# Kernel tuning notes

Measured on AMD Instinct MI355X. Metric: run time of the kernel, lower is better.

## Reference

```python
import jax, jax.numpy as jnp
import numpy as np

N, E = 50000, 800000
DIN, DOUT, DIM, K = 64, 64, 3, 8
EPS_GMM = 1e-15
BN_EPS = 1e-5
ALPHA = 0.01


def setup_inputs() -> dict:
    key = jax.random.key(0)
    ks = jax.random.split(key, 10)
    x = jax.random.normal(ks[0], (N, DIN), dtype=jnp.float32)
    edge_idx = jax.random.randint(ks[1], (2, E), 0, N, dtype=jnp.int64)
    edge_attr = jax.random.uniform(ks[2], (E, DIM), dtype=jnp.float32)
    # GMMConv params (PyG: g maps in -> K*out, lin is root weight, plus bias)
    W_g = jax.random.normal(ks[3], (DIN, K * DOUT), dtype=jnp.float32) * (1.0 / np.sqrt(DIN))
    mu = jax.random.normal(ks[4], (K, DIM), dtype=jnp.float32)
    sigma = jnp.ones((K, DIM), dtype=jnp.float32) + 0.1 * jax.random.normal(ks[5], (K, DIM), dtype=jnp.float32)
    W_root = jax.random.normal(ks[6], (DIN, DOUT), dtype=jnp.float32) * (1.0 / np.sqrt(DIN))
    bias = jnp.zeros((DOUT,), dtype=jnp.float32)
    gamma = jnp.ones((DOUT,), dtype=jnp.float32)
    beta = jnp.zeros((DOUT,), dtype=jnp.float32)
    return {"x": x, "edge_idx": edge_idx, "edge_attr": edge_attr,
            "W_g": W_g, "mu": mu, "sigma": sigma, "W_root": W_root,
            "bias": bias, "gamma": gamma, "beta": beta}


def reference(x, edge_idx, edge_attr, W_g, mu, sigma, W_root, bias, gamma, beta):
    src, dst = edge_idx[0], edge_idx[1]
    # Gaussian mixture edge weights: [E, K]
    diff = edge_attr[:, None, :] - mu[None, :, :]              # [E, K, DIM]
    gauss = jnp.exp((-0.5 * diff * diff / (EPS_GMM + sigma[None] ** 2)).sum(-1))  # [E, K]
    # Transform node features once: [N, K, DOUT]
    x_trans = (x @ W_g).reshape(N, K, DOUT)
    # Per-edge message: weighted sum over kernels of gathered source features
    msg = jnp.einsum('ekm,ek->em', x_trans[src], gauss)        # [E, DOUT]
    # Mean-aggregate to destination nodes
    agg = jax.ops.segment_sum(msg, dst, num_segments=N)        # [N, DOUT]
    cnt = jax.ops.segment_sum(jnp.ones((E,), dtype=x.dtype), dst, num_segments=N)
    agg = agg / jnp.maximum(cnt, 1.0)[:, None]
    # Root weight + bias
    out = agg + x @ W_root + bias
    # BatchNorm1d (training mode: batch stats, biased variance)
    m = out.mean(axis=0)
    v = ((out - m) ** 2).mean(axis=0)
    out = gamma * (out - m) * jax.lax.rsqrt(v + BN_EPS) + beta
    # LeakyReLU
    return jnp.where(out > 0, out, ALPHA * out)
```

## Files before the change

kernel.cpp:

```cpp
#include <hip/hip_runtime.h>
#include <hip/hip_bf16.h>

#define N_NODES 50000
#define N_EDGES 800000

__device__ __forceinline__ void store_val(float* p, float v) { *p = v; }
__device__ __forceinline__ void store_val(__hip_bfloat16* p, float v) { *p = __float2bfloat16(v); }
__device__ __forceinline__ float load_val(const float* p) { return *p; }
__device__ __forceinline__ float load_val(const __hip_bfloat16* p) { return __bfloat162float(*p); }

__global__ void prep_c1_kernel(const float* __restrict__ sigma, float* __restrict__ c1) {
    int i = threadIdx.x;
    if (i < 24) {
        float s = sigma[i];
        c1[i] = -0.5f / (s * s + 1e-15f);
    }
}

template <typename T>
__global__ void gemm_xt_kernel(const float* __restrict__ x, const float* __restrict__ Wg,
                               T* __restrict__ xt) {
    __shared__ float xs[16][64];
    const int tid = threadIdx.x;
    const int row0 = blockIdx.x << 4;
    for (int i = tid; i < 1024; i += 256) xs[i >> 6][i & 63] = x[(size_t)row0 * 64 + i];
    __syncthreads();

    float acc0[16], acc1[16];
#pragma unroll
    for (int r = 0; r < 16; r++) { acc0[r] = 0.f; acc1[r] = 0.f; }

#pragma unroll 4
    for (int i = 0; i < 64; i++) {
        float w0 = Wg[i * 512 + tid];
        float w1 = Wg[i * 512 + tid + 256];
#pragma unroll
        for (int r = 0; r < 16; r++) {
            float xv = xs[r][i];
            acc0[r] = fmaf(xv, w0, acc0[r]);
            acc1[r] = fmaf(xv, w1, acc1[r]);
        }
    }
#pragma unroll
    for (int r = 0; r < 16; r++) {
        size_t o = ((size_t)(row0 + r)) * 512 + tid;
        store_val(&xt[o], acc0[r]);
        store_val(&xt[o + 256], acc1[r]);
    }
}

template <typename T>
__global__ void edge_kernel(const int* __restrict__ eidx, const float* __restrict__ eattr,
                            const float* __restrict__ mu, const float* __restrict__ c1,
                            const T* __restrict__ xt, float* __restrict__ agg,
                            float* __restrict__ cnt) {
    __shared__ float smu[24], sc1[24];
    const int tid = threadIdx.x;
    if (tid < 24) smu[tid] = mu[tid];
    else if (tid < 48) sc1[tid - 24] = c1[tid - 24];
    __syncthreads();

    const int e = (blockIdx.x << 2) + (tid >> 6);
    const int lane = tid & 63;

    const int src = eidx[e];
    const int dst = eidx[N_EDGES + e];

    const float a0 = eattr[e * 3 + 0];
    const float a1 = eattr[e * 3 + 1];
    const float a2 = eattr[e * 3 + 2];

    const int kk = lane & 7;
    const float d0 = a0 - smu[kk * 3 + 0];
    const float d1 = a1 - smu[kk * 3 + 1];
    const float d2 = a2 - smu[kk * 3 + 2];
    const float gv = __expf(fmaf(d0 * d0, sc1[kk * 3 + 0],
                            fmaf(d1 * d1, sc1[kk * 3 + 1],
                                 d2 * d2 * sc1[kk * 3 + 2])));

    const T* xr = xt + (size_t)src * 512 + lane;
    float xv[8];
#pragma unroll
    for (int k = 0; k < 8; k++) xv[k] = load_val(&xr[k * 64]);

    float v = 0.f;
#pragma unroll
    for (int k = 0; k < 8; k++) {
        float gk = __shfl(gv, k, 64);
        v = fmaf(gk, xv[k], v);
    }

    atomicAdd(&agg[(size_t)dst * 64 + lane], v);
    if (lane == 0) atomicAdd(&cnt[dst], 1.0f);
}

__global__ void root_stats_kernel(const float* __restrict__ x, const float* __restrict__ Wr,
                                  const float* __restrict__ bias, const float* __restrict__ agg,
                                  const float* __restrict__ cnt, float* __restrict__ out_pre,
                                  double* __restrict__ colsum, double* __restrict__ colsumsq) {
    __shared__ float wr[4096];
    __shared__ float rs[256], rsq[256];
    for (int i = threadIdx.x; i < 4096; i += 256) wr[i] = Wr[i];
    __syncthreads();

    const int wave = threadIdx.x >> 6;
    const int lane = threadIdx.x & 63;
    const float b = bias[lane];
    const int stride = gridDim.x * 4;

    float s = 0.f, sq = 0.f;
    for (int n = blockIdx.x * 4 + wave; n < N_NODES; n += stride) {
        float xv = x[(size_t)n * 64 + lane];
        float acc = 0.f;
#pragma unroll
        for (int i = 0; i < 64; i++)
            acc = fmaf(__shfl(xv, i, 64), wr[i * 64 + lane], acc);
        float c = cnt[n];
        float val = agg[(size_t)n * 64 + lane] / fmaxf(c, 1.f) + acc + b;
        out_pre[(size_t)n * 64 + lane] = val;
        s += val;
        sq += val * val;
    }

    rs[threadIdx.x] = s;
    rsq[threadIdx.x] = sq;
    __syncthreads();
    if (threadIdx.x < 64) {
        float ts = rs[threadIdx.x] + rs[threadIdx.x + 64] + rs[threadIdx.x + 128] + rs[threadIdx.x + 192];
        float tq = rsq[threadIdx.x] + rsq[threadIdx.x + 64] + rsq[threadIdx.x + 128] + rsq[threadIdx.x + 192];
        atomicAdd(&colsum[threadIdx.x], (double)ts);
        atomicAdd(&colsumsq[threadIdx.x], (double)tq);
    }
}

__global__ void bn_prep_kernel(const double* __restrict__ colsum, const double* __restrict__ colsumsq,
                               float* __restrict__ meanr) {
    int c = threadIdx.x;
    if (c < 64) {
        double m = colsum[c] / (double)N_NODES;
        double var = colsumsq[c] / (double)N_NODES - m * m;
        meanr[c] = (float)m;
        meanr[64 + c] = (float)(1.0 / sqrt(var + 1e-5));
    }
}

__global__ void finalize_kernel(float* __restrict__ out, const float* __restrict__ meanr,
                                const float* __restrict__ gamma, const float* __restrict__ beta) {
    const int i = blockIdx.x * 256 + threadIdx.x;
    const int c = i & 63;
    float v = out[i];
    float o = fmaf((v - meanr[c]) * meanr[64 + c], gamma[c], beta[c]);
    out[i] = o > 0.f ? o : 0.01f * o;
}

extern "C" void kernel_launch(void* const* d_in, const int* in_sizes, int n_in,
                              void* d_out, int out_size, void* d_ws, size_t ws_size,
                              hipStream_t stream) {
    const float* x     = (const float*)d_in[0];
    const int*   eidx  = (const int*)d_in[1];
    const float* eattr = (const float*)d_in[2];
    const float* Wg    = (const float*)d_in[3];
    const float* mu    = (const float*)d_in[4];
    const float* sigma = (const float*)d_in[5];
    const float* Wr    = (const float*)d_in[6];
    const float* bias  = (const float*)d_in[7];
    const float* gamma = (const float*)d_in[8];
    const float* beta  = (const float*)d_in[9];
    float* out = (float*)d_out;

    char* ws = (char*)d_ws;
    const size_t agg_off     = 0;
    const size_t cnt_off     = agg_off + (size_t)N_NODES * 64 * 4;
    const size_t colsum_off  = cnt_off + (size_t)N_NODES * 4;
    const size_t colsumsq_off = colsum_off + 64 * 8;
    const size_t meanr_off   = colsumsq_off + 64 * 8;
    const size_t c1_off      = meanr_off + 128 * 4;
    const size_t xt_off      = c1_off + 128;
    const size_t zero_bytes  = colsumsq_off + 512;

    float*  agg      = (float*)(ws + agg_off);
    float*  cnt      = (float*)(ws + cnt_off);
    double* colsum   = (double*)(ws + colsum_off);
    double* colsumsq = (double*)(ws + colsumsq_off);
    float*  meanr    = (float*)(ws + meanr_off);
    float*  c1       = (float*)(ws + c1_off);

    hipMemsetAsync(ws + agg_off, 0, zero_bytes, stream);
    prep_c1_kernel<<<1, 32, 0, stream>>>(sigma, c1);

    const bool f32path = ws_size >= xt_off + (size_t)N_NODES * 512 * 4;
    if (f32path) {
        float* xt = (float*)(ws + xt_off);
        gemm_xt_kernel<float><<<N_NODES / 16, 256, 0, stream>>>(x, Wg, xt);
        edge_kernel<float><<<N_EDGES / 4, 256, 0, stream>>>(eidx, eattr, mu, c1, xt, agg, cnt);
    } else {
        __hip_bfloat16* xt = (__hip_bfloat16*)(ws + xt_off);
        gemm_xt_kernel<__hip_bfloat16><<<N_NODES / 16, 256, 0, stream>>>(x, Wg, xt);
        edge_kernel<__hip_bfloat16><<<N_EDGES / 4, 256, 0, stream>>>(eidx, eattr, mu, c1, xt, agg, cnt);
    }

    root_stats_kernel<<<1024, 256, 0, stream>>>(x, Wr, bias, agg, cnt, out, colsum, colsumsq);
    bn_prep_kernel<<<1, 64, 0, stream>>>(colsum, colsumsq, meanr);
    finalize_kernel<<<(N_NODES * 64) / 256, 256, 0, stream>>>(out, meanr, gamma, beta);
}
```

Measured before the change: 486.8 us.

## Group edges by source into CSR with precomputed weights, bf16 interleaved xt

Builds a source-sorted CSR (histogram, three-pass scan, scatter) so each wave loads a source node's transformed features once as a vectorized bf16 row, then loops over its outgoing edges using precomputed Gaussian weights already scaled by 1/indegree. xt is always stored in bf16 with a k-interleaved layout, which allows one 16-byte load per lane. The root/stats kernel is retiled into 16-row blocks that stage x in shared memory, and the mean division moves into the edge weights. This adds several preprocessing kernels and extra workspace traffic for gdst/gw, lowers xt precision, and keeps per-edge atomics onto dst.

Result: slower. 550.4 us (+13.1%).

```diff
diff --git a/kernel.cpp b/kernel.cpp
--- a/kernel.cpp
+++ b/kernel.cpp
@@ -3,11 +3,15 @@
 
 #define N_NODES 50000
 #define N_EDGES 800000
-
-__device__ __forceinline__ void store_val(float* p, float v) { *p = v; }
-__device__ __forceinline__ void store_val(__hip_bfloat16* p, float v) { *p = __float2bfloat16(v); }
-__device__ __forceinline__ float load_val(const float* p) { return *p; }
-__device__ __forceinline__ float load_val(const __hip_bfloat16* p) { return __bfloat162float(*p); }
+#define SCAN_BLOCK 512
+#define SCAN_GRID 98
+
+typedef __hip_bfloat16 bf16;
+
+__device__ __forceinline__ void store_g(float* p, float v) { *p = v; }
+__device__ __forceinline__ void store_g(bf16* p, float v) { *p = __float2bfloat16(v); }
+__device__ __forceinline__ float bf_lo(unsigned u) { union { unsigned i; float f; } c; c.i = u << 16; return c.f; }
+__device__ __forceinline__ float bf_hi(unsigned u) { union { unsigned i; float f; } c; c.i = u & 0xffff0000u; return c.f; }
 
 __global__ void prep_c1_kernel(const float* __restrict__ sigma, float* __restrict__ c1) {
     int i = threadIdx.x;
@@ -17,9 +21,8 @@
     }
 }
 
-template <typename T>
 __global__ void gemm_xt_kernel(const float* __restrict__ x, const float* __restrict__ Wg,
-                               T* __restrict__ xt) {
+                               bf16* __restrict__ xt) {
     __shared__ float xs[16][64];
     const int tid = threadIdx.x;
     const int row0 = blockIdx.x << 4;
@@ -41,31 +44,151 @@
             acc1[r] = fmaf(xv, w1, acc1[r]);
         }
     }
+    const int m = tid & 63, k0 = tid >> 6;
 #pragma unroll
     for (int r = 0; r < 16; r++) {
-        size_t o = ((size_t)(row0 + r)) * 512 + tid;
-        store_val(&xt[o], acc0[r]);
-        store_val(&xt[o + 256], acc1[r]);
-    }
-}
-
-template <typename T>
-__global__ void edge_kernel(const int* __restrict__ eidx, const float* __restrict__ eattr,
-                            const float* __restrict__ mu, const float* __restrict__ c1,
-                            const T* __restrict__ xt, float* __restrict__ agg,
-                            float* __restrict__ cnt) {
+        size_t base = ((size_t)(row0 + r)) * 512 + m * 8 + k0;
+        xt[base] = __float2bfloat16(acc0[r]);
+        xt[base + 4] = __float2bfloat16(acc1[r]);
+    }
+}
+
+__global__ void hist_kernel(const int* __restrict__ eidx, int* __restrict__ deg_src,
+                            int* __restrict__ indeg) {
+    const int e = blockIdx.x * 256 + threadIdx.x;
+    if (e < N_EDGES) {
+        atomicAdd(&deg_src[eidx[e]], 1);
+        atomicAdd(&indeg[eidx[N_EDGES + e]], 1);
+    }
+}
+
+__global__ void scan1_kernel(const int* __restrict__ deg, int* __restrict__ excl,
+                             int* __restrict__ bsum) {
+    __shared__ int sd[SCAN_BLOCK];
+    const int tid = threadIdx.x;
+    const int i = blockIdx.x * SCAN_BLOCK + tid;
+    const int v = (i < N_NODES) ? deg[i] : 0;
+    sd[tid] = v;
+    for (int off = 1; off < SCAN_BLOCK; off <<= 1) {
+        __syncthreads();
+        const int t = (tid >= off) ? sd[tid - off] : 0;
+        __syncthreads();
+        sd[tid] += t;
+    }
+    if (i < N_NODES) excl[i] = sd[tid] - v;
+    if (tid == SCAN_BLOCK - 1) bsum[blockIdx.x] = sd[tid];
+}
+
+__global__ void scan2_kernel(const int* __restrict__ bsum, int* __restrict__ boff,
+                             int* __restrict__ starts) {
+    if (threadIdx.x == 0) {
+        int acc = 0;
+        for (int b = 0; b < SCAN_GRID; ++b) { boff[b] = acc; acc += bsum[b]; }
+        starts[N_NODES] = acc;
+    }
+}
+
+__global__ void scan3_kernel(const int* __restrict__ excl, const int* __restrict__ boff,
+                             int* __restrict__ starts, int* __restrict__ cursor) {
+    const int i = blockIdx.x * SCAN_BLOCK + threadIdx.x;
+    if (i < N_NODES) {
+        const int s = excl[i] + boff[blockIdx.x];
+        starts[i] = s;
+        cursor[i] = s;
+    }
+}
+
+template <typename GT>
+__global__ void build_kernel(const int* __restrict__ eidx, const float* __restrict__ eattr,
+                             const float* __restrict__ mu, const float* __restrict__ c1,
+                             const int* __restrict__ indeg, int* __restrict__ cursor,
+                             int* __restrict__ gdst, GT* __restrict__ gw) {
     __shared__ float smu[24], sc1[24];
     const int tid = threadIdx.x;
     if (tid < 24) smu[tid] = mu[tid];
     else if (tid < 48) sc1[tid - 24] = c1[tid - 24];
     __syncthreads();
 
+    const int e = blockIdx.x * 256 + tid;
+    if (e >= N_EDGES) return;
+    const int src = eidx[e];
+    const int dst = eidx[N_EDGES + e];
+    const float a0 = eattr[3 * e + 0];
+    const float a1 = eattr[3 * e + 1];
+    const float a2 = eattr[3 * e + 2];
+    const int dg = indeg[dst];
+    const float inv = 1.0f / (float)(dg > 1 ? dg : 1);
+
+    const int pos = atomicAdd(&cursor[src], 1);
+    gdst[pos] = dst;
+    GT* gp = gw + (size_t)pos * 8;
+#pragma unroll
+    for (int k = 0; k < 8; k++) {
+        const float d0 = a0 - smu[3 * k + 0];
+        const float d1 = a1 - smu[3 * k + 1];
+        const float d2 = a2 - smu[3 * k + 2];
+        const float g = __expf(fmaf(d0 * d0, sc1[3 * k + 0],
+                               fmaf(d1 * d1, sc1[3 * k + 1],
+                                    d2 * d2 * sc1[3 * k + 2])));
+        store_g(&gp[k], g * inv);
+    }
+}
+
+template <typename GT>
+__global__ void __launch_bounds__(256) csr_kernel(const int* __restrict__ starts,
+                                                  const int* __restrict__ gdst,
+                                                  const GT* __restrict__ gw,
+                                                  const bf16* __restrict__ xt,
+                                                  float* __restrict__ agg) {
+    const int wid = (blockIdx.x << 2) + (threadIdx.x >> 6);
+    const int lane = threadIdx.x & 63;
+    if (wid >= N_NODES) return;
+    const int s0 = starts[wid], s1 = starts[wid + 1];
+    if (s0 >= s1) return;
+
+    const int4 q = *(const int4*)(xt + (size_t)wid * 512 + lane * 8);
+    float xv[8];
+    xv[0] = bf_lo(q.x); xv[1] = bf_hi(q.x);
+    xv[2] = bf_lo(q.y); xv[3] = bf_hi(q.y);
+    xv[4] = bf_lo(q.z); xv[5] = bf_hi(q.z);
+    xv[6] = bf_lo(q.w); xv[7] = bf_hi(q.w);
+
+    for (int j = s0; j < s1; ++j) {
+        const int dst = gdst[j];
+        float g[8];
+        if constexpr (sizeof(GT) == 4) {
+            const float4 g0 = *(const float4*)(gw + (size_t)j * 8);
+            const float4 g1 = *(const float4*)(gw + (size_t)j * 8 + 4);
+            g[0] = g0.x; g[1] = g0.y; g[2] = g0.z; g[3] = g0.w;
+            g[4] = g1.x; g[5] = g1.y; g[6] = g1.z; g[7] = g1.w;
+        } else {
+            const int4 gq = *(const int4*)(gw + (size_t)j * 8);
+            g[0] = bf_lo(gq.x); g[1] = bf_hi(gq.x);
+            g[2] = bf_lo(gq.y); g[3] = bf_hi(gq.y);
+            g[4] = bf_lo(gq.z); g[5] = bf_hi(gq.z);
+            g[6] = bf_lo(gq.w); g[7] = bf_hi(gq.w);
+        }
+        float v = 0.f;
+#pragma unroll
+        for (int k = 0; k < 8; k++) v = fmaf(g[k], xv[k], v);
+        atomicAdd(&agg[(size_t)dst * 64 + lane], v);
+    }
+}
+
+__global__ void edge_fallback_kernel(const int* __restrict__ eidx, const float* __restrict__ eattr,
+                                     const float* __restrict__ mu, const float* __restrict__ c1,
+                                     const bf16* __restrict__ xt, float* __restrict__ agg,
+                                     float* __restrict__ cnt) {
+    __shared__ float smu[24], sc1[24];
+    const int tid = threadIdx.x;
+    if (tid < 24) smu[tid] = mu[tid];
+    else if (tid < 48) sc1[tid - 24] = c1[tid - 24];
+    __syncthreads();
+
     const int e = (blockIdx.x << 2) + (tid >> 6);
     const int lane = tid & 63;
-
     const int src = eidx[e];
     const int dst = eidx[N_EDGES + e];
-
     const float a0 = eattr[e * 3 + 0];
     const float a1 = eattr[e * 3 + 1];
     const float a2 = eattr[e * 3 + 2];
@@ -78,10 +201,12 @@
                             fmaf(d1 * d1, sc1[kk * 3 + 1],
                                  d2 * d2 * sc1[kk * 3 + 2])));
 
-    const T* xr = xt + (size_t)src * 512 + lane;
+    const int4 q = *(const int4*)(xt + (size_t)src * 512 + lane * 8);
     float xv[8];
-#pragma unroll
-    for (int k = 0; k < 8; k++) xv[k] = load_val(&xr[k * 64]);
+    xv[0] = bf_lo(q.x); xv[1] = bf_hi(q.x);
+    xv[2] = bf_lo(q.y); xv[3] = bf_hi(q.y);
+    xv[4] = bf_lo(q.z); xv[5] = bf_hi(q.z);
+    xv[6] = bf_lo(q.w); xv[7] = bf_hi(q.w);
 
     float v = 0.f;
 #pragma unroll
@@ -89,56 +214,59 @@
         float gk = __shfl(gv, k, 64);
         v = fmaf(gk, xv[k], v);
     }
-
     atomicAdd(&agg[(size_t)dst * 64 + lane], v);
     if (lane == 0) atomicAdd(&cnt[dst], 1.0f);
 }
 
+__global__ void divide_kernel(float* __restrict__ agg, const float* __restrict__ cnt) {
+    const int i = blockIdx.x * 256 + threadIdx.x;
+    agg[i] /= fmaxf(cnt[i >> 6], 1.0f);
+}
+
 __global__ void root_stats_kernel(const float* __restrict__ x, const float* __restrict__ Wr,
                                   const float* __restrict__ bias, const float* __restrict__ agg,
-                                  const float* __restrict__ cnt, float* __restrict__ out_pre,
+                                  float* __restrict__ out,
                                   double* __restrict__ colsum, double* __restrict__ colsumsq) {
     __shared__ float wr[4096];
+    __shared__ float xs[16][64];
     __shared__ float rs[256], rsq[256];
-    for (int i = threadIdx.x; i < 4096; i += 256) wr[i] = Wr[i];
-    __syncthreads();
-
-    const int wave = threadIdx.x >> 6;
-    const int lane = threadIdx.x & 63;
-    const float b = bias[lane];
-    const int stride = gridDim.x * 4;
-
+    const int tid = threadIdx.x;
+    for (int i = tid; i < 4096; i += 256) wr[i] = Wr[i];
+    const int row0 = blockIdx.x << 4;
+    for (int i = tid; i < 1024; i += 256) xs[i >> 6][i & 63] = x[(size_t)row0 * 64 + i];
+    __syncthreads();
+
+    const int col = tid & 63, rg = tid >> 6;
+    const float b = bias[col];
     float s = 0.f, sq = 0.f;
-    for (int n = blockIdx.x * 4 + wave; n < N_NODES; n += stride) {
-        float xv = x[(size_t)n * 64 + lane];
+#pragma unroll
+    for (int rr = 0; rr < 4; rr++) {
+        const int r = rg * 4 + rr;
         float acc = 0.f;
 #pragma unroll
-        for (int i = 0; i < 64; i++)
-            acc = fmaf(__shfl(xv, i, 64), wr[i * 64 + lane], acc);
-        float c = cnt[n];
-        float val = agg[(size_t)n * 64 + lane] / fmaxf(c, 1.f) + acc + b;
-        out_pre[(size_t)n * 64 + lane] = val;
+        for (int i = 0; i < 64; i++) acc = fmaf(xs[r][i], wr[i * 64 + col], acc);
+        const size_t o = (size_t)(row0 + r) * 64 + col;
+        const float val = agg[o] + acc + b;
+        out[o] = val;
         s += val;
         sq += val * val;
     }
-
-    rs[threadIdx.x] = s;
-    rsq[threadIdx.x] = sq;
-    __syncthreads();
-    if (threadIdx.x < 64) {
-        float ts = rs[threadIdx.x] + rs[threadIdx.x + 64] + rs[threadIdx.x + 128] + rs[threadIdx.x + 192];
-        float tq = rsq[threadIdx.x] + rsq[threadIdx.x + 64] + rsq[threadIdx.x + 128] + rsq[threadIdx.x + 192];
-        atomicAdd(&colsum[threadIdx.x], (double)ts);
-        atomicAdd(&colsumsq[threadIdx.x], (double)tq);
+    rs[tid] = s; rsq[tid] = sq;
+    __syncthreads();
+    if (tid < 64) {
+        const float ts = rs[tid] + rs[tid + 64] + rs[tid + 128] + rs[tid + 192];
+        const float tq = rsq[tid] + rsq[tid + 64] + rsq[tid + 128] + rsq[tid + 192];
+        atomicAdd(&colsum[tid], (double)ts);
+        atomicAdd(&colsumsq[tid], (double)tq);
     }
 }
 
 __global__ void bn_prep_kernel(const double* __restrict__ colsum, const double* __restrict__ colsumsq,
                                float* __restrict__ meanr) {
-    int c = threadIdx.x;
+    const int c = threadIdx.x;
     if (c < 64) {
-        double m = colsum[c] / (double)N_NODES;
-        double var = colsumsq[c] / (double)N_NODES - m * m;
+        const double m = colsum[c] / (double)N_NODES;
+        const double var = colsumsq[c] / (double)N_NODES - m * m;
         meanr[c] = (float)m;
         meanr[64 + c] = (float)(1.0 / sqrt(var + 1e-5));
     }
@@ -148,8 +276,8 @@
                                 const float* __restrict__ gamma, const float* __restrict__ beta) {
     const int i = blockIdx.x * 256 + threadIdx.x;
     const int c = i & 63;
-    float v = out[i];
-    float o = fmaf((v - meanr[c]) * meanr[64 + c], gamma[c], beta[c]);
+    const float v = out[i];
+    const float o = fmaf((v - meanr[c]) * meanr[64 + c], gamma[c], beta[c]);
     out[i] = o > 0.f ? o : 0.01f * o;
 }
 
@@ -169,37 +297,71 @@
     float* out = (float*)d_out;
 
     char* ws = (char*)d_ws;
-    const size_t agg_off     = 0;
-    const size_t cnt_off     = agg_off + (size_t)N_NODES * 64 * 4;
-    const size_t colsum_off  = cnt_off + (size_t)N_NODES * 4;
-    const size_t colsumsq_off = colsum_off + 64 * 8;
-    const size_t meanr_off   = colsumsq_off + 64 * 8;
-    const size_t c1_off      = meanr_off + 128 * 4;
-    const size_t xt_off      = c1_off + 128;
-    const size_t zero_bytes  = colsumsq_off + 512;
+    const size_t agg_off      = 0;
+    const size_t indeg_off    = 12800000;
+    const size_t degsrc_off   = 13000000;
+    const size_t colsum_off   = 13200000;
+    const size_t colsumsq_off = 13200512;
+    const size_t zero_bytes   = 13201024;
+    const size_t meanr_off    = 13201024;
+    const size_t c1_off       = 13201536;
+    const size_t excl_off     = 13201664;
+    const size_t bsum_off     = 13401664;
+    const size_t boff_off     = 13402176;
+    const size_t starts_off   = 13402688;
+    const size_t cursor_off   = 13602752;
+    const size_t gdst_off     = 13802752;
+    const size_t gw_off       = 17002752;
+    const size_t planA_xt_off = gw_off + (size_t)N_EDGES * 8 * 4;
+    const size_t planB_xt_off = gw_off + (size_t)N_EDGES * 8 * 2;
+    const size_t fb_xt_off    = 13201664;
+    const size_t xt_bytes     = (size_t)N_NODES * 512 * 2;
 
     float*  agg      = (float*)(ws + agg_off);
-    float*  cnt      = (float*)(ws + cnt_off);
+    int*    indeg    = (int*)(ws + indeg_off);
+    float*  cnt      = (float*)(ws + indeg_off);
+    int*    deg_src  = (int*)(ws + degsrc_off);
     double* colsum   = (double*)(ws + colsum_off);
     double* colsumsq = (double*)(ws + colsumsq_off);
     float*  meanr    = (float*)(ws + meanr_off);
     float*  c1       = (float*)(ws + c1_off);
+    int*    excl     = (int*)(ws + excl_off);
+    int*    bsum     = (int*)(ws + bsum_off);
+    int*    boff     = (int*)(ws + boff_off);
+    int*    starts   = (int*)(ws + starts_off);
+    int*    cursor   = (int*)(ws + cursor_off);
+    int*    gdst     = (int*)(ws + gdst_off);
 
     hipMemsetAsync(ws + agg_off, 0, zero_bytes, stream);
     prep_c1_kernel<<<1, 32, 0, stream>>>(sigma, c1);
 
-    const bool f32path = ws_size >= xt_off + (size_t)N_NODES * 512 * 4;
-    if (f32path) {
-        float* xt = (float*)(ws + xt_off);
-        gemm_xt_kernel<float><<<N_NODES / 16, 256, 0, stream>>>(x, Wg, xt);
-        edge_kernel<float><<<N_EDGES / 4, 256, 0, stream>>>(eidx, eattr, mu, c1, xt, agg, cnt);
+    const bool planA = ws_size >= planA_xt_off + xt_bytes;
+    const bool planB = !planA && ws_size >= planB_xt_off + xt_bytes;
+
+    if (planA || planB) {
+        bf16* xt = (bf16*)(ws + (planA ? planA_xt_off : planB_xt_off));
+        gemm_xt_kernel<<<N_NODES / 16, 256, 0, stream>>>(x, Wg, xt);
+        hist_kernel<<<N_EDGES / 256, 256, 0, stream>>>(eidx, deg_src, indeg);
+        scan1_kernel<<<SCAN_GRID, SCAN_BLOCK, 0, stream>>>(deg_src, excl, bsum);
+        scan2_kernel<<<1, 64, 0, stream>>>(bsum, boff, starts);
+        scan3_kernel<<<SCAN_GRID, SCAN_BLOCK, 0, stream>>>(excl, boff, starts, cursor);
+        if (planA) {
+            float* gw = (float*)(ws + gw_off);
+            build_kernel<float><<<N_EDGES / 256, 256, 0, stream>>>(eidx, eattr, mu, c1, indeg, cursor, gdst, gw);
+            csr_kernel<float><<<N_NODES / 4, 256, 0, stream>>>(starts, gdst, gw, xt, agg);
+        } else {
+            bf16* gw = (bf16*)(ws + gw_off);
+            build_kernel<bf16><<<N_EDGES / 256, 256, 0, stream>>>(eidx, eattr, mu, c1, indeg, cursor, gdst, gw);
+            csr_kernel<bf16><<<N_NODES / 4, 256, 0, stream>>>(starts, gdst, gw, xt, agg);
+        }
     } else {
-        __hip_bfloat16* xt = (__hip_bfloat16*)(ws + xt_off);
-        gemm_xt_kernel<__hip_bfloat16><<<N_NODES / 16, 256, 0, stream>>>(x, Wg, xt);
-        edge_kernel<__hip_bfloat16><<<N_EDGES / 4, 256, 0, stream>>>(eidx, eattr, mu, c1, xt, agg, cnt);
-    }
-
-    root_stats_kernel<<<1024, 256, 0, stream>>>(x, Wr, bias, agg, cnt, out, colsum, colsumsq);
+        bf16* xt = (bf16*)(ws + fb_xt_off);
+        gemm_xt_kernel<<<N_NODES / 16, 256, 0, stream>>>(x, Wg, xt);
+        edge_fallback_kernel<<<N_EDGES / 4, 256, 0, stream>>>(eidx, eattr, mu, c1, xt, agg, cnt);
+        divide_kernel<<<(N_NODES * 64) / 256, 256, 0, stream>>>(agg, cnt);
+    }
+
+    root_stats_kernel<<<N_NODES / 16, 256, 0, stream>>>(x, Wr, bias, agg, out, colsum, colsumsq);
     bn_prep_kernel<<<1, 64, 0, stream>>>(colsum, colsumsq, meanr);
     finalize_kernel<<<(N_NODES * 64) / 256, 256, 0, stream>>>(out, meanr, gamma, beta);
 }
```

## Sort edges by source into CSR and aggregate per-source with bf16 xt

Applied to the files above, without the earlier changes.

Builds a source-sorted edge list each call (histogram, single-block scan, and atomic cursor scatter), packing the eight Gaussian weights per edge as bf16 plus a 16-bit destination index. A per-source-node wave then loads its bf16 transformed row once and scatters weighted messages to destinations with atomics. This replaces the per-edge gather of a full 512-wide row. xt is now always bf16 in a kernel-interleaved layout, and the degree count comes from an integer in-degree histogram. The root GEMM is restructured to stage x tiles in shared memory. The trade-off is several extra passes and a serial scan, plus reduced precision in the gathered features and edge weights.

Result: slower. 662.6 us (+36.1%).

```diff
diff --git a/kernel.cpp b/kernel.cpp
--- a/kernel.cpp
+++ b/kernel.cpp
@@ -3,11 +3,17 @@
 
 #define N_NODES 50000
 #define N_EDGES 800000
-
-__device__ __forceinline__ void store_val(float* p, float v) { *p = v; }
-__device__ __forceinline__ void store_val(__hip_bfloat16* p, float v) { *p = __float2bfloat16(v); }
-__device__ __forceinline__ float load_val(const float* p) { return *p; }
-__device__ __forceinline__ float load_val(const __hip_bfloat16* p) { return __bfloat162float(*p); }
+#define SCAN_T 1024
+#define CHUNK 49
+
+typedef __hip_bfloat16 bf16;
+
+__device__ __forceinline__ float bf_lo(unsigned u) { union { unsigned i; float f; } c; c.i = u << 16; return c.f; }
+__device__ __forceinline__ float bf_hi(unsigned u) { union { unsigned i; float f; } c; c.i = u & 0xffff0000u; return c.f; }
+__device__ __forceinline__ unsigned short bfbits(float f) {
+    bf16 b = __float2bfloat16(f);
+    union { bf16 b; unsigned short u; } c; c.b = b; return c.u;
+}
 
 __global__ void prep_c1_kernel(const float* __restrict__ sigma, float* __restrict__ c1) {
     int i = threadIdx.x;
@@ -17,9 +23,8 @@
     }
 }
 
-template <typename T>
 __global__ void gemm_xt_kernel(const float* __restrict__ x, const float* __restrict__ Wg,
-                               T* __restrict__ xt) {
+                               bf16* __restrict__ xt) {
     __shared__ float xs[16][64];
     const int tid = threadIdx.x;
     const int row0 = blockIdx.x << 4;
@@ -41,104 +46,188 @@
             acc1[r] = fmaf(xv, w1, acc1[r]);
         }
     }
+    const int m = tid & 63, k0 = tid >> 6;
 #pragma unroll
     for (int r = 0; r < 16; r++) {
-        size_t o = ((size_t)(row0 + r)) * 512 + tid;
-        store_val(&xt[o], acc0[r]);
-        store_val(&xt[o + 256], acc1[r]);
-    }
-}
-
-template <typename T>
-__global__ void edge_kernel(const int* __restrict__ eidx, const float* __restrict__ eattr,
-                            const float* __restrict__ mu, const float* __restrict__ c1,
-                            const T* __restrict__ xt, float* __restrict__ agg,
-                            float* __restrict__ cnt) {
+        size_t base = ((size_t)(row0 + r)) * 512 + m * 8 + k0;
+        xt[base] = __float2bfloat16(acc0[r]);
+        xt[base + 4] = __float2bfloat16(acc1[r]);
+    }
+}
+
+__global__ void hist_kernel(const int* __restrict__ eidx, int* __restrict__ deg_src,
+                            int* __restrict__ indeg) {
+    const int t = blockIdx.x * 256 + threadIdx.x;
+    const int e0 = t * 4;
+    if (e0 >= N_EDGES) return;
+    const int4 s4 = *(const int4*)(eidx + e0);
+    const int4 d4 = *(const int4*)(eidx + N_EDGES + e0);
+    atomicAdd(&deg_src[s4.x], 1); atomicAdd(&deg_src[s4.y], 1);
+    atomicAdd(&deg_src[s4.z], 1); atomicAdd(&deg_src[s4.w], 1);
+    atomicAdd(&indeg[d4.x], 1);   atomicAdd(&indeg[d4.y], 1);
+    atomicAdd(&indeg[d4.z], 1);   atomicAdd(&indeg[d4.w], 1);
+}
+
+__global__ void scan_kernel(const int* __restrict__ deg, int* __restrict__ starts,
+                            int* __restrict__ cursor) {
+    __shared__ int part[SCAN_T];
+    const int t = threadIdx.x;
+    const int base = t * CHUNK;
+    int s = 0;
+    for (int i = 0; i < CHUNK; i++) {
+        const int idx = base + i;
+        if (idx < N_NODES) s += deg[idx];
+    }
+    part[t] = s;
+    __syncthreads();
+    for (int off = 1; off < SCAN_T; off <<= 1) {
+        const int v = (t >= off) ? part[t - off] : 0;
+        __syncthreads();
+        part[t] += v;
+        __syncthreads();
+    }
+    int run = part[t] - s;
+    for (int i = 0; i < CHUNK; i++) {
+        const int idx = base + i;
+        if (idx < N_NODES) {
+            starts[idx] = run;
+            cursor[idx] = run;
+            run += deg[idx];
+        }
+    }
+    if (t == SCAN_T - 1) starts[N_NODES] = run;
+}
+
+__global__ void build_kernel(const int* __restrict__ eidx, const float* __restrict__ eattr,
+                             const float* __restrict__ mu, const float* __restrict__ c1,
+                             int* __restrict__ cursor, unsigned short* __restrict__ gdst,
+                             int4* __restrict__ gwv) {
     __shared__ float smu[24], sc1[24];
     const int tid = threadIdx.x;
     if (tid < 24) smu[tid] = mu[tid];
     else if (tid < 48) sc1[tid - 24] = c1[tid - 24];
     __syncthreads();
 
-    const int e = (blockIdx.x << 2) + (tid >> 6);
-    const int lane = tid & 63;
-
+    const int e = blockIdx.x * 256 + tid;
+    if (e >= N_EDGES) return;
     const int src = eidx[e];
     const int dst = eidx[N_EDGES + e];
-
-    const float a0 = eattr[e * 3 + 0];
-    const float a1 = eattr[e * 3 + 1];
-    const float a2 = eattr[e * 3 + 2];
-
-    const int kk = lane & 7;
-    const float d0 = a0 - smu[kk * 3 + 0];
-    const float d1 = a1 - smu[kk * 3 + 1];
-    const float d2 = a2 - smu[kk * 3 + 2];
-    const float gv = __expf(fmaf(d0 * d0, sc1[kk * 3 + 0],
-                            fmaf(d1 * d1, sc1[kk * 3 + 1],
-                                 d2 * d2 * sc1[kk * 3 + 2])));
-
-    const T* xr = xt + (size_t)src * 512 + lane;
+    const float a0 = eattr[3 * e + 0];
+    const float a1 = eattr[3 * e + 1];
+    const float a2 = eattr[3 * e + 2];
+
+    unsigned short h[8];
+#pragma unroll
+    for (int k = 0; k < 8; k++) {
+        const float d0 = a0 - smu[3 * k + 0];
+        const float d1 = a1 - smu[3 * k + 1];
+        const float d2 = a2 - smu[3 * k + 2];
+        const float g = __expf(fmaf(d0 * d0, sc1[3 * k + 0],
+                               fmaf(d1 * d1, sc1[3 * k + 1],
+                                    d2 * d2 * sc1[3 * k + 2])));
+        h[k] = bfbits(g);
+    }
+    const int pos = atomicAdd(&cursor[src], 1);
+    int4 q;
+    q.x = (int)h[0] | ((int)h[1] << 16);
+    q.y = (int)h[2] | ((int)h[3] << 16);
+    q.z = (int)h[4] | ((int)h[5] << 16);
+    q.w = (int)h[6] | ((int)h[7] << 16);
+    gwv[pos] = q;
+    gdst[pos] = (unsigned short)dst;
+}
+
+__global__ void __launch_bounds__(256) csr_kernel(const int* __restrict__ starts,
+                                                  const unsigned short* __restrict__ gdst,
+                                                  const int4* __restrict__ gwv,
+                                                  const bf16* __restrict__ xt,
+                                                  float* __restrict__ agg) {
+    const int wid = (blockIdx.x << 2) + (threadIdx.x >> 6);
+    const int lane = threadIdx.x & 63;
+    const int s0 = starts[wid], s1 = starts[wid + 1];
+    if (s0 >= s1) return;
+
+    const int4 q = *(const int4*)(xt + (size_t)wid * 512 + lane * 8);
     float xv[8];
-#pragma unroll
-    for (int k = 0; k < 8; k++) xv[k] = load_val(&xr[k * 64]);
-
-    float v = 0.f;
-#pragma unroll
-    for (int k = 0; k < 8; k++) {
-        float gk = __shfl(gv, k, 64);
-        v = fmaf(gk, xv[k], v);
-    }
-
-    atomicAdd(&agg[(size_t)dst * 64 + lane], v);
-    if (lane == 0) atomicAdd(&cnt[dst], 1.0f);
+    xv[0] = bf_lo(q.x); xv[1] = bf_hi(q.x);
+    xv[2] = bf_lo(q.y); xv[3] = bf_hi(q.y);
+    xv[4] = bf_lo(q.z); xv[5] = bf_hi(q.z);
+    xv[6] = bf_lo(q.w); xv[7] = bf_hi(q.w);
+
+    int j = s0;
+    for (; j + 2 <= s1; j += 2) {
+        const int4 g0 = gwv[j];
+        const int4 g1 = gwv[j + 1];
+        const int d0 = gdst[j];
+        const int d1 = gdst[j + 1];
+        float v0 = bf_lo(g0.x) * xv[0] + bf_hi(g0.x) * xv[1]
+                 + bf_lo(g0.y) * xv[2] + bf_hi(g0.y) * xv[3]
+                 + bf_lo(g0.z) * xv[4] + bf_hi(g0.z) * xv[5]
+                 + bf_lo(g0.w) * xv[6] + bf_hi(g0.w) * xv[7];
+        atomicAdd(&agg[(size_t)d0 * 64 + lane], v0);
+        float v1 = bf_lo(g1.x) * xv[0] + bf_hi(g1.x) * xv[1]
+                 + bf_lo(g1.y) * xv[2] + bf_hi(g1.y) * xv[3]
+                 + bf_lo(g1.z) * xv[4] + bf_hi(g1.z) * xv[5]
+                 + bf_lo(g1.w) * xv[6] + bf_hi(g1.w) * xv[7];
+        atomicAdd(&agg[(size_t)d1 * 64 + lane], v1);
+    }
+    if (j < s1) {
+        const int4 g0 = gwv[j];
+        const int d0 = gdst[j];
+        float v0 = bf_lo(g0.x) * xv[0] + bf_hi(g0.x) * xv[1]
+                 + bf_lo(g0.y) * xv[2] + bf_hi(g0.y) * xv[3]
+                 + bf_lo(g0.z) * xv[4] + bf_hi(g0.z) * xv[5]
+                 + bf_lo(g0.w) * xv[6] + bf_hi(g0.w) * xv[7];
+        atomicAdd(&agg[(size_t)d0 * 64 + lane], v0);
+    }
 }
 
 __global__ void root_stats_kernel(const float* __restrict__ x, const float* __restrict__ Wr,
                                   const float* __restrict__ bias, const float* __restrict__ agg,
-                                  const float* __restrict__ cnt, float* __restrict__ out_pre,
+                                  const int* __restrict__ indeg, float* __restrict__ out,
                                   double* __restrict__ colsum, double* __restrict__ colsumsq) {
     __shared__ float wr[4096];
+    __shared__ float xs[16][64];
     __shared__ float rs[256], rsq[256];
-    for (int i = threadIdx.x; i < 4096; i += 256) wr[i] = Wr[i];
-    __syncthreads();
-
-    const int wave = threadIdx.x >> 6;
-    const int lane = threadIdx.x & 63;
-    const float b = bias[lane];
-    const int stride = gridDim.x * 4;
-
+    const int tid = threadIdx.x;
+    for (int i = tid; i < 4096; i += 256) wr[i] = Wr[i];
+    const int row0 = blockIdx.x << 4;
+    for (int i = tid; i < 1024; i += 256) xs[i >> 6][i & 63] = x[(size_t)row0 * 64 + i];
+    __syncthreads();
+
+    const int col = tid & 63, rg = tid >> 6;
+    const float b = bias[col];
     float s = 0.f, sq = 0.f;
-    for (int n = blockIdx.x * 4 + wave; n < N_NODES; n += stride) {
-        float xv = x[(size_t)n * 64 + lane];
+#pragma unroll
+    for (int rr = 0; rr < 4; rr++) {
+        const int r = rg * 4 + rr;
+        const int node = row0 + r;
         float acc = 0.f;
 #pragma unroll
-        for (int i = 0; i < 64; i++)
-            acc = fmaf(__shfl(xv, i, 64), wr[i * 64 + lane], acc);
-        float c = cnt[n];
-        float val = agg[(size_t)n * 64 + lane] / fmaxf(c, 1.f) + acc + b;
-        out_pre[(size_t)n * 64 + lane] = val;
+        for (int i = 0; i < 64; i++) acc = fmaf(xs[r][i], wr[i * 64 + col], acc);
+        const size_t o = (size_t)node * 64 + col;
+        const float inv = 1.0f / fmaxf((float)indeg[node], 1.0f);
+        const float val = agg[o] * inv + acc + b;
+        out[o] = val;
         s += val;
         sq += val * val;
     }
-
-    rs[threadIdx.x] = s;
-    rsq[threadIdx.x] = sq;
-    __syncthreads();
-    if (threadIdx.x < 64) {
-        float ts = rs[threadIdx.x] + rs[threadIdx.x + 64] + rs[threadIdx.x + 128] + rs[threadIdx.x + 192];
-        float tq = rsq[threadIdx.x] + rsq[threadIdx.x + 64] + rsq[threadIdx.x + 128] + rsq[threadIdx.x + 192];
-        atomicAdd(&colsum[threadIdx.x], (double)ts);
-        atomicAdd(&colsumsq[threadIdx.x], (double)tq);
+    rs[tid] = s; rsq[tid] = sq;
+    __syncthreads();
+    if (tid < 64) {
+        const float ts = rs[tid] + rs[tid + 64] + rs[tid + 128] + rs[tid + 192];
+        const float tq = rsq[tid] + rsq[tid + 64] + rsq[tid + 128] + rsq[tid + 192];
+        atomicAdd(&colsum[tid], (double)ts);
+        atomicAdd(&colsumsq[tid], (double)tq);
     }
 }
 
 __global__ void bn_prep_kernel(const double* __restrict__ colsum, const double* __restrict__ colsumsq,
                                float* __restrict__ meanr) {
-    int c = threadIdx.x;
+    const int c = threadIdx.x;
     if (c < 64) {
-        double m = colsum[c] / (double)N_NODES;
-        double var = colsumsq[c] / (double)N_NODES - m * m;
+        const double m = colsum[c] / (double)N_NODES;
+        const double var = colsumsq[c] / (double)N_NODES - m * m;
         meanr[c] = (float)m;
         meanr[64 + c] = (float)(1.0 / sqrt(var + 1e-5));
     }
@@ -148,8 +237,8 @@
                                 const float* __restrict__ gamma, const float* __restrict__ beta) {
     const int i = blockIdx.x * 256 + threadIdx.x;
     const int c = i & 63;
-    float v = out[i];
-    float o = fmaf((v - meanr[c]) * meanr[64 + c], gamma[c], beta[c]);
+    const float v = out[i];
+    const float o = fmaf((v - meanr[c]) * meanr[64 + c], gamma[c], beta[c]);
     out[i] = o > 0.f ? o : 0.01f * o;
 }
 
@@ -169,37 +258,41 @@
     float* out = (float*)d_out;
 
     char* ws = (char*)d_ws;
-    const size_t agg_off     = 0;
-    const size_t cnt_off     = agg_off + (size_t)N_NODES * 64 * 4;
-    const size_t colsum_off  = cnt_off + (size_t)N_NODES * 4;
-    const size_t colsumsq_off = colsum_off + 64 * 8;
-    const size_t meanr_off   = colsumsq_off + 64 * 8;
-    const size_t c1_off      = meanr_off + 128 * 4;
-    const size_t xt_off      = c1_off + 128;
-    const size_t zero_bytes  = colsumsq_off + 512;
-
-    float*  agg      = (float*)(ws + agg_off);
-    float*  cnt      = (float*)(ws + cnt_off);
-    double* colsum   = (double*)(ws + colsum_off);
-    double* colsumsq = (double*)(ws + colsumsq_off);
-    float*  meanr    = (float*)(ws + meanr_off);
-    float*  c1       = (float*)(ws + c1_off);
+    const size_t agg_off      = 0;
+    const size_t degsrc_off   = 12800000;
+    const size_t indeg_off    = 13000000;
+    const size_t colsum_off   = 13200000;
+    const size_t colsumsq_off = 13200512;
+    const size_t zero_bytes   = 13201024;
+    const size_t c1_off       = 13201024;
+    const size_t meanr_off    = 13201152;
+    const size_t sstarts_off  = 13201664;
+    const size_t cursor_off   = 13401728;
+    const size_t gdst_off     = 13601728;
+    const size_t gw_off       = 15201728;
+    const size_t xt_off       = 28001728;
+
+    float*          agg      = (float*)(ws + agg_off);
+    int*            deg_src  = (int*)(ws + degsrc_off);
+    int*            indeg    = (int*)(ws + indeg_off);
+    double*         colsum   = (double*)(ws + colsum_off);
+    double*         colsumsq = (double*)(ws + colsumsq_off);
+    float*          c1       = (float*)(ws + c1_off);
+    float*          meanr    = (float*)(ws + meanr_off);
+    int*            sstarts  = (int*)(ws + sstarts_off);
+    int*            cursor   = (int*)(ws + cursor_off);
+    unsigned short* gdst     = (unsigned short*)(ws + gdst_off);
+    int4*           gwv      = (int4*)(ws + gw_off);
+    bf16*           xt       = (bf16*)(ws + xt_off);
 
     hipMemsetAsync(ws + agg_off, 0, zero_bytes, stream);
     prep_c1_kernel<<<1, 32, 0, stream>>>(sigma, c1);
-
-    const bool f32path = ws_size >= xt_off + (size_t)N_NODES * 512 * 4;
-    if (f32path) {
-        float* xt = (float*)(ws + xt_off);
-        gemm_xt_kernel<float><<<N_NODES / 16, 256, 0, stream>>>(x, Wg, xt);
-        edge_kernel<float><<<N_EDGES / 4, 256, 0, stream>>>(eidx, eattr, mu, c1, xt, agg, cnt);
-    } else {
-        __hip_bfloat16* xt = (__hip_bfloat16*)(ws + xt_off);
-        gemm_xt_kernel<__hip_bfloat16><<<N_NODES / 16, 256, 0, stream>>>(x, Wg, xt);
-        edge_kernel<__hip_bfloat16><<<N_EDGES / 4, 256, 0, stream>>>(eidx, eattr, mu, c1, xt, agg, cnt);
-    }
-
-    root_stats_kernel<<<1024, 256, 0, stream>>>(x, Wr, bias, agg, cnt, out, colsum, colsumsq);
+    gemm_xt_kernel<<<N_NODES / 16, 256, 0, stream>>>(x, Wg, xt);
+    hist_kernel<<<(N_EDGES / 4 + 255) / 256, 256, 0, stream>>>(eidx, deg_src, indeg);
+    scan_kernel<<<1, SCAN_T, 0, stream>>>(deg_src, sstarts, cursor);
+    build_kernel<<<N_EDGES / 256, 256, 0, stream>>>(eidx, eattr, mu, c1, cursor, gdst, gwv);
+    csr_kernel<<<N_NODES / 4, 256, 0, stream>>>(sstarts, gdst, gwv, xt, agg);
+    root_stats_kernel<<<N_NODES / 16, 256, 0, stream>>>(x, Wr, bias, agg, indeg, out, colsum, colsumsq);
     bn_prep_kernel<<<1, 64, 0, stream>>>(colsum, colsumsq, meanr);
     finalize_kernel<<<(N_NODES * 64) / 256, 256, 0, stream>>>(out, meanr, gamma, beta);
 }
```
